# Kernel optimization log

Hardware: AMD Instinct MI355X
Metric: run time of the kernel (lower is better)

The kernel has to match this reference:

```python
import jax, jax.numpy as jnp
import numpy as np

ALPHA = 2.0  # init alpha
B, N, E = 8, 100000, 3200000


def setup_inputs() -> dict:
    key = jax.random.key(0)
    k1, k2, k3, k4 = jax.random.split(key, 4)
    y = jax.random.normal(k1, (B, N), dtype=jnp.float32)
    t = jnp.zeros((1,), dtype=jnp.float32)  # unused by the math, kept for signature fidelity
    graph_edge_attr = jax.random.uniform(k2, (E,), dtype=jnp.float32)
    dist_w = jax.random.normal(k3, (E,), dtype=jnp.float32)  # distances.weight ([E,1] flattened)
    edge_index = jax.random.randint(k4, (2, E), 0, N, dtype=jnp.int64)
    return {"y": y, "t": t, "graph_edge_attr": graph_edge_attr, "dist_w": dist_w, "edge_index": edge_index}


def reference(y, t, graph_edge_attr, dist_w, edge_index):
    ei0 = edge_index[0]  # source node per edge [E]
    ei1 = edge_index[1]  # target node per edge [E]
    n = y.shape[1]
    # edge_attr = sigmoid(distances.weight) -> [E]
    edge_attr = jax.nn.sigmoid(dist_w)
    # deg = scatter_add(graph.edge_attr, edge_index[0], dim_size=N) -> [N]
    deg = jax.ops.segment_sum(graph_edge_attr, ei0, num_segments=n)
    deg_a = jnp.power(deg[ei0], ALPHA)  # [E], gathered per edge at source node
    # grad_m = sqrt(edge_attr) * -1 * min(y[:,ei1]/deg^a - y[:,ei0]/deg^a, 0) -> [B,E]
    diff = y[:, ei1] / deg_a - y[:, ei0] / deg_a
    grad_m = jnp.sqrt(edge_attr) * (-1.0) * jnp.minimum(diff, 0.0)
    # grad_norm = scatter_add(|grad_m|, ei0, dim=1, dim_size=N) -> [B,N]
    grad_norm = jnp.zeros_like(y).at[:, ei0].add(jnp.abs(grad_m))
    # run_pde is None -> return f (mask branch not taken)
    return 1.0 - grad_norm
```

## Files before the change

kernel.cpp:

```cpp
#include <hip/hip_runtime.h>
#include <hip/hip_fp16.h>

#define BATCH 8
#define S_LOG 9
#define SBUCKET 512
#define KC 256
#define CB 1024
#define TTILE 2048
#define EPT 8
#define MA 8

static inline size_t alignup(size_t x) { return (x + 255) & ~(size_t)255; }

__device__ __forceinline__ unsigned bf16hi(unsigned u) {
    return (u + 0x7FFFu + ((u >> 16) & 1u)) >> 16;
}

__device__ __forceinline__ int aligned_chunk(int E) {
    return (((E + CB - 1) / CB) + 15) & ~15;
}


__global__ __launch_bounds__(256)
void count_transpose_kernel(const int* __restrict__ ei0, unsigned* __restrict__ counts,
                            const float* __restrict__ y, uint4* __restrict__ yT,
                            int E, int N, int Npad) {
    __shared__ unsigned cnt[KC];
    int tid = threadIdx.x;
    if (blockIdx.x >= CB) {
        int n = (blockIdx.x - CB) * 256 + tid;
        if (n < Npad) {
            uint4 o = make_uint4(0u, 0u, 0u, 0u);
            if (n < N) {
                unsigned p[8];
#pragma unroll
                for (int b = 0; b < BATCH; ++b)
                    p[b] = bf16hi(__float_as_uint(y[(size_t)b * N + n]));
                o = make_uint4(p[0] | (p[1] << 16), p[2] | (p[3] << 16),
                               p[4] | (p[5] << 16), p[6] | (p[7] << 16));
            }
            yT[n] = o;
        }
        return;
    }
    cnt[tid] = 0;
    __syncthreads();
    int chunk = aligned_chunk(E);
    int lo = blockIdx.x * chunk;
    int hi = min(lo + chunk, E);
    for (int bi = lo; bi < hi; bi += 1024) {
        int idx = bi + tid * 4;
        if (idx + 4 <= hi) {
            int4 v = *(const int4*)(ei0 + idx);
            atomicAdd(&cnt[(unsigned)v.x >> S_LOG], 1u);
            atomicAdd(&cnt[(unsigned)v.y >> S_LOG], 1u);
            atomicAdd(&cnt[(unsigned)v.z >> S_LOG], 1u);
            atomicAdd(&cnt[(unsigned)v.w >> S_LOG], 1u);
        } else {
#pragma unroll
            for (int j = 0; j < 4; ++j) {
                int i2 = idx + j;
                if (i2 < hi) atomicAdd(&cnt[(unsigned)ei0[i2] >> S_LOG], 1u);
            }
        }
    }
    __syncthreads();
    counts[(size_t)tid * CB + blockIdx.x] = cnt[tid];
}

__global__ __launch_bounds__(256)
void scanB1_kernel(const unsigned* __restrict__ counts, unsigned* __restrict__ base,
                   unsigned* __restrict__ tot) {
    __shared__ unsigned ssum[256];
    int k = blockIdx.x, tid = threadIdx.x;
    const uint4* row4 = (const uint4*)(counts + (size_t)k * CB);
    uint4 v = row4[tid];
    unsigned lsum = v.x + v.y + v.z + v.w;
    ssum[tid] = lsum;
    __syncthreads();
    for (int off = 1; off < 256; off <<= 1) {
        unsigned u = ssum[tid];
        unsigned a = (tid >= off) ? ssum[tid - off] : 0u;
        __syncthreads();
        ssum[tid] = u + a;
        __syncthreads();
    }
    unsigned ex = ssum[tid] - lsum;
    if (tid == 255) tot[k] = ssum[255];
    uint4 o;
    o.x = ex;
    o.y = ex + v.x;
    o.z = o.y + v.y;
    o.w = o.z + v.z;
    ((uint4*)(base + (size_t)k * CB))[tid] = o;
}

__global__ void scanC_kernel(const unsigned* __restrict__ tot,
                             unsigned* __restrict__ bb, int E, int K) {
    __shared__ unsigned sb[KC];
    int t = threadIdx.x;
    unsigned v = (t < K) ? tot[t] : 0u;
    sb[t] = v;
    __syncthreads();
    for (int off = 1; off < KC; off <<= 1) {
        unsigned u = sb[t];
        unsigned a = (t >= off) ? sb[t - off] : 0u;
        __syncthreads();
        sb[t] = u + a;
        __syncthreads();
    }
    bb[t] = sb[t] - v;
    if (t == KC - 1) bb[KC] = (unsigned)E;
}

__global__ __launch_bounds__(256)
void scatter_kernel(const int* __restrict__ ei0, const int* __restrict__ ei1,
                    const float* __restrict__ dw, const float* __restrict__ gea,
                    const unsigned* __restrict__ base, const unsigned* __restrict__ bb,
                    uint2* __restrict__ w0coef, int E) {
    __shared__ unsigned cursor[KC];
    __shared__ unsigned h[KC];
    __shared__ unsigned tstart[KC];
    __shared__ unsigned wsum[4];
    __shared__ uint2 srec[TTILE];
    __shared__ unsigned char skey[TTILE];
    int tid = threadIdx.x;
    cursor[tid] = base[(size_t)tid * CB + blockIdx.x] + bb[tid];
    int chunk = aligned_chunk(E);
    int lo = blockIdx.x * chunk;
    int hi = min(lo + chunk, E);
    __syncthreads();

    for (int tileLo = lo; tileLo < hi; tileLo += TTILE) {
        int tn = min(TTILE, hi - tileLo);
        h[tid] = 0;
        __syncthreads();

        int base_off = tid * EPT;
        unsigned k_r[EPT], w0_r[EPT], pk_r[EPT], rk_r[EPT];
        int s0a[EPT], s1a[EPT];
        float dwa[EPT], gea_a[EPT];
        bool anyv = base_off < tn;
        if (base_off + EPT <= tn) {
            const int4* p0 = (const int4*)(ei0 + tileLo + base_off);
            const int4* p1 = (const int4*)(ei1 + tileLo + base_off);
            const float4* pd = (const float4*)(dw + tileLo + base_off);
            const float4* pg = (const float4*)(gea + tileLo + base_off);
            int4 a0 = p0[0], a1 = p0[1];
            int4 b0 = p1[0], b1 = p1[1];
            float4 d0 = pd[0], d1 = pd[1];
            float4 g0 = pg[0], g1 = pg[1];
            s0a[0]=a0.x; s0a[1]=a0.y; s0a[2]=a0.z; s0a[3]=a0.w;
            s0a[4]=a1.x; s0a[5]=a1.y; s0a[6]=a1.z; s0a[7]=a1.w;
            s1a[0]=b0.x; s1a[1]=b0.y; s1a[2]=b0.z; s1a[3]=b0.w;
            s1a[4]=b1.x; s1a[5]=b1.y; s1a[6]=b1.z; s1a[7]=b1.w;
            dwa[0]=d0.x; dwa[1]=d0.y; dwa[2]=d0.z; dwa[3]=d0.w;
            dwa[4]=d1.x; dwa[5]=d1.y; dwa[6]=d1.z; dwa[7]=d1.w;
            gea_a[0]=g0.x; gea_a[1]=g0.y; gea_a[2]=g0.z; gea_a[3]=g0.w;
            gea_a[4]=g1.x; gea_a[5]=g1.y; gea_a[6]=g1.z; gea_a[7]=g1.w;
#pragma unroll
            for (int j = 0; j < EPT; ++j) k_r[j] = 0u;
#pragma unroll
            for (int j = 0; j < EPT; ++j) {
                unsigned k = (unsigned)s0a[j] >> S_LOG;
                unsigned s0l = (unsigned)(s0a[j] & (SBUCKET - 1));
                k_r[j] = k;
                w0_r[j] = (unsigned)s1a[j] | (s0l << 17);
                float sig = 1.0f / (1.0f + __expf(-dwa[j]));
                pk_r[j] = (bf16hi(__float_as_uint(sqrtf(sig))) << 16) |
                          bf16hi(__float_as_uint(gea_a[j]));
            }
#pragma unroll
            for (int j = 0; j < EPT; ++j)
                rk_r[j] = atomicAdd(&h[k_r[j]], 1u);
        } else {
#pragma unroll
            for (int j = 0; j < EPT; ++j) {
                int off = base_off + j;
                k_r[j] = 0xFFFFFFFFu;
                if (off < tn) {
                    int i = tileLo + off;
                    int s0v = ei0[i];
                    int s1v = ei1[i];
                    unsigned k = (unsigned)s0v >> S_LOG;
                    unsigned s0l = (unsigned)(s0v & (SBUCKET - 1));
                    k_r[j] = k;
                    w0_r[j] = (unsigned)s1v | (s0l << 17);
                    float sig = 1.0f / (1.0f + __expf(-dw[i]));
                    pk_r[j] = (bf16hi(__float_as_uint(sqrtf(sig))) << 16) |
                              bf16hi(__float_as_uint(gea[i]));
                }
            }
#pragma unroll
            for (int j = 0; j < EPT; ++j)
                if (k_r[j] != 0xFFFFFFFFu) rk_r[j] = atomicAdd(&h[k_r[j]], 1u);
        }
        bool fullv = base_off + EPT <= tn;
        __syncthreads();

        unsigned hv = h[tid];
        unsigned v = hv;
        unsigned lane = tid & 63;
        unsigned wv = tid >> 6;
#pragma unroll
        for (int off = 1; off < 64; off <<= 1) {
            unsigned t = __shfl_up(v, off, 64);
            if (lane >= off) v += t;
        }
        if (lane == 63) wsum[wv] = v;
        __syncthreads();
        unsigned addv = 0;
#pragma unroll
        for (unsigned w = 0; w < 4; ++w)
            if (w < wv) addv += wsum[w];
        tstart[tid] = v + addv - hv;
        __syncthreads();

        if (fullv) {
#pragma unroll
            for (int j = 0; j < EPT; ++j) {
                unsigned slot = tstart[k_r[j]] + rk_r[j];
                srec[slot] = make_uint2(w0_r[j], pk_r[j]);
                skey[slot] = (unsigned char)k_r[j];
            }
        } else if (anyv) {
#pragma unroll
            for (int j = 0; j < EPT; ++j)
                if (k_r[j] != 0xFFFFFFFFu) {
                    unsigned slot = tstart[k_r[j]] + rk_r[j];
                    srec[slot] = make_uint2(w0_r[j], pk_r[j]);
                    skey[slot] = (unsigned char)k_r[j];
                }
        }
        __syncthreads();

        for (int i = tid; i < tn; i += 256) {
            uint2 u = srec[i];
            unsigned k = skey[i];
            unsigned pos = cursor[k] + ((unsigned)i - tstart[k]);
            w0coef[pos] = u;
        }
        __syncthreads();
        cursor[tid] += h[tid];
        __syncthreads();
    }
}

__global__ __launch_bounds__(128)
void accum_kernel(const uint2* __restrict__ w0coef, const unsigned* __restrict__ bb,
                  const uint4* __restrict__ yT,
                  float* __restrict__ pdegp, __half2* __restrict__ pout,
                  int N, int Npad) {
    __shared__ uint4  outw[2][SBUCKET];
    __shared__ float  degw[2][SBUCKET];
    int k = blockIdx.x, m = blockIdx.y, tid = threadIdx.x;
    int n0 = k << S_LOG;
    unsigned lane = tid & 63;
    unsigned wv = tid >> 6;

    uint4 z4i = make_uint4(0u, 0u, 0u, 0u);
    for (int i = tid; i < 2 * SBUCKET; i += 128)
        ((uint4*)outw)[i] = z4i;
    for (int i = tid; i < 2 * SBUCKET; i += 128)
        ((float*)degw)[i] = 0.0f;
    unsigned lo = bb[k], hi = bb[k + 1];
    unsigned cnt = hi - lo;
    unsigned slice = (cnt + MA - 1) / MA;
    unsigned slo = lo + m * slice;
    unsigned shi = min(slo + slice, hi);
    __syncthreads();

    uint4* myout = outw[wv];
    float* mydeg = degw[wv];

    unsigned i0 = slo + tid;
    uint2 z2 = make_uint2(0u, 0u);
    uint2 c0 = z2, c1 = z2, d0 = z2, d1 = z2;
    uint4 zg = make_uint4(0u, 0u, 0u, 0u);
    uint4 g0 = zg, g1 = zg, yg0 = zg, yg1 = zg;
    bool vc0 = i0 < shi,       vc1 = i0 + 128 < shi;
    bool vd0 = i0 + 256 < shi, vd1 = i0 + 384 < shi;
    if (vc0) c0 = w0coef[i0];
    if (vc1) c1 = w0coef[i0 + 128];
    if (vd0) d0 = w0coef[i0 + 256];
    if (vd1) d1 = w0coef[i0 + 384];
    if (vc0) { g0 = yT[c0.x & 0x1FFFFu]; yg0 = yT[n0 + (c0.x >> 17)]; }
    if (vc1) { g1 = yT[c1.x & 0x1FFFFu]; yg1 = yT[n0 + (c1.x >> 17)]; }

    while (__any(vc0)) {
        uint4 h0 = zg, h1 = zg, yh0 = zg, yh1 = zg;
        if (vd0) { h0 = yT[d0.x & 0x1FFFFu]; yh0 = yT[n0 + (d0.x >> 17)]; }
        if (vd1) { h1 = yT[d1.x & 0x1FFFFu]; yh1 = yT[n0 + (d1.x >> 17)]; }
        uint2 e0 = z2, e1 = z2;
        bool ve0 = i0 + 512 < shi, ve1 = i0 + 640 < shi;
        if (ve0) e0 = w0coef[i0 + 512];
        if (ve1) e1 = w0coef[i0 + 640];

#pragma unroll
        for (int half = 0; half < 2; ++half) {
            bool val = half ? vc1 : vc0;
            uint2 cc = half ? c1 : c0;
            uint4 gg = half ? g1 : g0;
            uint4 y0r = half ? yg1 : yg0;
            unsigned s0l = cc.x >> 17;
            unsigned long long mm = ~0ull;
#pragma unroll
            for (int b = 0; b < 9; ++b) {
                unsigned long long vb = __ballot((s0l >> b) & 1u);
                mm &= ((s0l >> b) & 1u) ? vb : ~vb;
            }
            unsigned rank = __popcll(mm & ((1ull << lane) - 1ull));
            float cf = __uint_as_float(cc.y & 0xFFFF0000u);
            float ge = __uint_as_float(cc.y << 16);
            float q[8];
            {
                const unsigned yw[4] = {y0r.x, y0r.y, y0r.z, y0r.w};
                const unsigned gw[4] = {gg.x, gg.y, gg.z, gg.w};
#pragma unroll
                for (int p = 0; p < 4; ++p) {
                    float ya = __uint_as_float(yw[p] << 16);
                    float yb = __uint_as_float(yw[p] & 0xFFFF0000u);
                    float ga = __uint_as_float(gw[p] << 16);
                    float gb = __uint_as_float(gw[p] & 0xFFFF0000u);
                    q[2 * p]     = cf * fmaxf(ya - ga, 0.0f);
                    q[2 * p + 1] = cf * fmaxf(yb - gb, 0.0f);
                }
            }
            unsigned r = 0;
            bool pending = val;
            while (__any(pending && rank >= r ? 1 : 0)) {
                if (pending && rank == r) {
                    uint4 cur = myout[s0l];
                    unsigned cw[4] = {cur.x, cur.y, cur.z, cur.w};
#pragma unroll
                    for (int p = 0; p < 4; ++p) {
                        __half2 hv = *reinterpret_cast<__half2*>(&cw[p]);
                        float2 f = __half22float2(hv);
                        f.x += q[2 * p];
                        f.y += q[2 * p + 1];
                        hv = __floats2half2_rn(f.x, f.y);
                        cw[p] = *reinterpret_cast<unsigned*>(&hv);
                    }
                    myout[s0l] = make_uint4(cw[0], cw[1], cw[2], cw[3]);
                    mydeg[s0l] += ge;
                    pending = false;
                }
                ++r;
            }
        }

        c0 = d0; c1 = d1; d0 = e0; d1 = e1;
        g0 = h0; g1 = h1; yg0 = yh0; yg1 = yh1;
        vc0 = vd0; vc1 = vd1; vd0 = ve0; vd1 = ve1;
        i0 += 256;
    }
    __syncthreads();

    for (int i = tid; i < SBUCKET; i += 128)
        pdegp[(size_t)m * Npad + n0 + i] = degw[0][i] + degw[1][i];
    for (int j = tid; j < SBUCKET; j += 128) {
        uint4 a = outw[0][j];
        uint4 b = outw[1][j];
        unsigned aw[4] = {a.x, a.y, a.z, a.w};
        unsigned bw[4] = {b.x, b.y, b.z, b.w};
#pragma unroll
        for (int p = 0; p < 4; ++p) {
            float2 fa = __half22float2(*reinterpret_cast<__half2*>(&aw[p]));
            float2 fb = __half22float2(*reinterpret_cast<__half2*>(&bw[p]));
            pout[((size_t)m * 4 + p) * Npad + n0 + j] =
                __floats2half2_rn(fa.x + fb.x, fa.y + fb.y);
        }
    }
}

__global__ __launch_bounds__(256)
void finalize_kernel(const float* __restrict__ pdegp, const __half2* __restrict__ pout,
                     float* __restrict__ out, int N, int Npad) {
    int n = blockIdx.x * blockDim.x + threadIdx.x;
    if (n >= N) return;
    float d = 0.0f;
#pragma unroll
    for (int m = 0; m < MA; ++m) d += pdegp[(size_t)m * Npad + n];
    float inv = 1.0f / (d * d);
#pragma unroll
    for (int p = 0; p < 4; ++p) {
        float sx = 0.0f, sy = 0.0f;
#pragma unroll
        for (int m = 0; m < MA; ++m) {
            float2 f = __half22float2(pout[((size_t)m * 4 + p) * Npad + n]);
            sx += f.x; sy += f.y;
        }
        out[(size_t)(2 * p) * N + n]     = 1.0f - sx * inv;
        out[(size_t)(2 * p + 1) * N + n] = 1.0f - sy * inv;
    }
}


__global__ void fill_one_kernel(float* __restrict__ out, int n) {
    int i = blockIdx.x * blockDim.x + threadIdx.x;
    if (i < n) out[i] = 1.0f;
}

__global__ void zero_kernel(float* __restrict__ p, int n) {
    int i = blockIdx.x * blockDim.x + threadIdx.x;
    if (i < n) p[i] = 0.0f;
}

__global__ void deg_kernel(const float* __restrict__ gea,
                           const int* __restrict__ ei0,
                           float* __restrict__ deg, int E) {
    int e = blockIdx.x * blockDim.x + threadIdx.x;
    if (e < E) atomicAdd(&deg[ei0[e]], gea[e]);
}

__global__ void edge_kernel(const float* __restrict__ y,
                            const float* __restrict__ dw,
                            const int* __restrict__ ei0,
                            const int* __restrict__ ei1,
                            const float* __restrict__ deg,
                            float* __restrict__ out,
                            int E, int N) {
    int e = blockIdx.x * blockDim.x + threadIdx.x;
    if (e >= E) return;
    int s0 = ei0[e];
    int s1 = ei1[e];
    float d = deg[s0];
    float inv = 1.0f / (d * d);
    float sig = 1.0f / (1.0f + __expf(-dw[e]));
    float coef = sqrtf(sig) * inv;
#pragma unroll
    for (int b = 0; b < BATCH; ++b) {
        float y0 = y[(size_t)b * N + s0];
        float y1 = y[(size_t)b * N + s1];
        float gm = coef * fmaxf(y0 - y1, 0.0f);
        if (gm != 0.0f) atomicAdd(&out[(size_t)b * N + s0], -gm);
    }
}


extern "C" void kernel_launch(void* const* d_in, const int* in_sizes, int n_in,
                              void* d_out, int out_size, void* d_ws, size_t ws_size,
                              hipStream_t stream) {
    const float* y   = (const float*)d_in[0];
    const float* gea = (const float*)d_in[2];
    const float* dw  = (const float*)d_in[3];
    const int*   ei  = (const int*)d_in[4];

    const int E = in_sizes[2];
    const int N = in_sizes[0] / BATCH;
    const int* ei0 = ei;
    const int* ei1 = ei + E;

    const int K = (N + SBUCKET - 1) >> S_LOG;
    const int Npad = K << S_LOG;

    size_t o_yT     = 0;
    size_t o_rcf    = o_yT     + alignup((size_t)Npad * 16);
    size_t o_counts = o_rcf    + alignup((size_t)E * 8);
    size_t o_base   = o_counts + alignup((size_t)KC * CB * 4);
    size_t o_tot    = o_base   + alignup((size_t)KC * CB * 4);
    size_t o_bb     = o_tot    + alignup((size_t)KC * 4);
    size_t o_pdegp  = o_bb     + alignup((size_t)(KC + 1) * 4);
    size_t o_pout   = o_pdegp  + alignup((size_t)MA * Npad * 4);
    size_t need     = o_pout   + alignup((size_t)MA * 4 * Npad * 4);

    if (K <= KC && N <= 131071 && ws_size >= need) {
        char* w = (char*)d_ws;
        uint4*    yT     = (uint4*)(w + o_yT);
        uint2*    w0coef = (uint2*)(w + o_rcf);
        unsigned* counts = (unsigned*)(w + o_counts);
        unsigned* base   = (unsigned*)(w + o_base);
        unsigned* tot    = (unsigned*)(w + o_tot);
        unsigned* bb     = (unsigned*)(w + o_bb);
        float*    pdegp  = (float*)(w + o_pdegp);
        __half2*  pout   = (__half2*)(w + o_pout);

        int tb = (Npad + 255) / 256;
        count_transpose_kernel<<<CB + tb, 256, 0, stream>>>(ei0, counts, y, yT,
                                                            E, N, Npad);
        scanB1_kernel<<<K, 256, 0, stream>>>(counts, base, tot);
        scanC_kernel<<<1, KC, 0, stream>>>(tot, bb, E, K);
        scatter_kernel<<<CB, 256, 0, stream>>>(ei0, ei1, dw, gea, base, bb,
                                               w0coef, E);
        accum_kernel<<<dim3(K, MA), 128, 0, stream>>>(w0coef, bb, yT,
                                                      pdegp, pout, N, Npad);
        finalize_kernel<<<(N + 255) / 256, 256, 0, stream>>>(
            pdegp, pout, (float*)d_out, N, Npad);
    } else {
        float* deg = (float*)d_ws;
        zero_kernel<<<(N + 255) / 256, 256, 0, stream>>>(deg, N);
        fill_one_kernel<<<(out_size + 255) / 256, 256, 0, stream>>>((float*)d_out, out_size);
        deg_kernel<<<(E + 255) / 256, 256, 0, stream>>>(gea, ei0, deg, E);
        edge_kernel<<<(E + 255) / 256, 256, 0, stream>>>(y, dw, ei0, ei1, deg,
                                                         (float*)d_out, E, N);
    }
}
```

Baseline: 159.9 us.

## Defer duplicate-slot updates to shared overflow queue instead of serialized rank loop

In the per-bucket accumulation loop, only the first lane targeting each slot updates shared memory directly. Lanes that collide are pushed into a per-wave shared overflow queue and processed in batches later with the rank-serialized path, which re-gathers yT for them. This removes the wave-wide serialization loop from the common path at the cost of extra LDS, atomics and re-gathers for duplicates. MA is also reduced from 8 to 6, giving fewer edge slices per bucket.

```diff
diff --git a/kernel.cpp b/kernel.cpp
--- a/kernel.cpp
+++ b/kernel.cpp
@@ -8,7 +8,8 @@
 #define CB 1024
 #define TTILE 2048
 #define EPT 8
-#define MA 8
+#define MA 6
+#define QCAP 384
 
 static inline size_t alignup(size_t x) { return (x + 255) & ~(size_t)255; }
 
@@ -246,6 +247,61 @@
     }
 }
 
+__device__ __forceinline__ void process_dups(uint4* myout, float* mydeg,
+                                             const uint4* __restrict__ yT, int n0,
+                                             uint2 cc, bool val, unsigned lane) {
+    unsigned s0l = cc.x >> 17;
+    unsigned long long mm = ~0ull;
+#pragma unroll
+    for (int b = 0; b < 9; ++b) {
+        unsigned long long vb = __ballot((s0l >> b) & 1u);
+        mm &= ((s0l >> b) & 1u) ? vb : ~vb;
+    }
+    {
+        unsigned long long vb = __ballot(val ? 1 : 0);
+        mm &= val ? vb : ~vb;
+    }
+    unsigned rank = __popcll(mm & ((1ull << lane) - 1ull));
+    uint4 zg = make_uint4(0u, 0u, 0u, 0u);
+    uint4 gg = zg, y0r = zg;
+    if (val) { gg = yT[cc.x & 0x1FFFFu]; y0r = yT[n0 + s0l]; }
+    float cf = __uint_as_float(cc.y & 0xFFFF0000u);
+    float ge = __uint_as_float(cc.y << 16);
+    float q[8];
+    const unsigned yw[4] = {y0r.x, y0r.y, y0r.z, y0r.w};
+    const unsigned gw[4] = {gg.x, gg.y, gg.z, gg.w};
+#pragma unroll
+    for (int p = 0; p < 4; ++p) {
+        float ya = __uint_as_float(yw[p] << 16);
+        float yb = __uint_as_float(yw[p] & 0xFFFF0000u);
+        float ga = __uint_as_float(gw[p] << 16);
+        float gb = __uint_as_float(gw[p] & 0xFFFF0000u);
+        q[2 * p]     = cf * fmaxf(ya - ga, 0.0f);
+        q[2 * p + 1] = cf * fmaxf(yb - gb, 0.0f);
+    }
+    unsigned r = 0;
+    bool pending = val;
+    while (__any(pending && rank >= r ? 1 : 0)) {
+        if (pending && rank == r) {
+            uint4 cur = myout[s0l];
+            unsigned cw[4] = {cur.x, cur.y, cur.z, cur.w};
+#pragma unroll
+            for (int p = 0; p < 4; ++p) {
+                __half2 hv = *reinterpret_cast<__half2*>(&cw[p]);
+                float2 f = __half22float2(hv);
+                f.x += q[2 * p];
+                f.y += q[2 * p + 1];
+                hv = __floats2half2_rn(f.x, f.y);
+                cw[p] = *reinterpret_cast<unsigned*>(&hv);
+            }
+            myout[s0l] = make_uint4(cw[0], cw[1], cw[2], cw[3]);
+            mydeg[s0l] += ge;
+            pending = false;
+        }
+        ++r;
+    }
+}
+
 __global__ __launch_bounds__(128)
 void accum_kernel(const uint2* __restrict__ w0coef, const unsigned* __restrict__ bb,
                   const uint4* __restrict__ yT,
@@ -253,6 +309,8 @@
                   int N, int Npad) {
     __shared__ uint4  outw[2][SBUCKET];
     __shared__ float  degw[2][SBUCKET];
+    __shared__ uint2  ovq[2][QCAP];
+    __shared__ unsigned ovn[2];
     int k = blockIdx.x, m = blockIdx.y, tid = threadIdx.x;
     int n0 = k << S_LOG;
     unsigned lane = tid & 63;
@@ -263,6 +321,7 @@
         ((uint4*)outw)[i] = z4i;
     for (int i = tid; i < 2 * SBUCKET; i += 128)
         ((float*)degw)[i] = 0.0f;
+    if (tid < 2) ovn[tid] = 0u;
     unsigned lo = bb[k], hi = bb[k + 1];
     unsigned cnt = hi - lo;
     unsigned slice = (cnt + MA - 1) / MA;
@@ -288,6 +347,16 @@
     if (vc1) { g1 = yT[c1.x & 0x1FFFFu]; yg1 = yT[n0 + (c1.x >> 17)]; }
 
     while (__any(vc0)) {
+        if (ovn[wv] > (QCAP - 130)) {
+            unsigned qn = ovn[wv];
+            for (unsigned qb = 0; qb < qn; qb += 64) {
+                unsigned qidx = qb + lane;
+                uint2 qc = (qidx < qn) ? ovq[wv][qidx] : z2;
+                process_dups(myout, mydeg, yT, n0, qc, qidx < qn, lane);
+            }
+            if (lane == 0) ovn[wv] = 0u;
+        }
+
         uint4 h0 = zg, h1 = zg, yh0 = zg, yh1 = zg;
         if (vd0) { h0 = yT[d0.x & 0x1FFFFu]; yh0 = yT[n0 + (d0.x >> 17)]; }
         if (vd1) { h1 = yT[d1.x & 0x1FFFFu]; yh1 = yT[n0 + (d1.x >> 17)]; }
@@ -309,27 +378,27 @@
                 unsigned long long vb = __ballot((s0l >> b) & 1u);
                 mm &= ((s0l >> b) & 1u) ? vb : ~vb;
             }
+            {
+                unsigned long long vb = __ballot(val ? 1 : 0);
+                mm &= val ? vb : ~vb;
+            }
             unsigned rank = __popcll(mm & ((1ull << lane) - 1ull));
-            float cf = __uint_as_float(cc.y & 0xFFFF0000u);
-            float ge = __uint_as_float(cc.y << 16);
-            float q[8];
-            {
-                const unsigned yw[4] = {y0r.x, y0r.y, y0r.z, y0r.w};
-                const unsigned gw[4] = {gg.x, gg.y, gg.z, gg.w};
-#pragma unroll
-                for (int p = 0; p < 4; ++p) {
-                    float ya = __uint_as_float(yw[p] << 16);
-                    float yb = __uint_as_float(yw[p] & 0xFFFF0000u);
-                    float ga = __uint_as_float(gw[p] << 16);
-                    float gb = __uint_as_float(gw[p] & 0xFFFF0000u);
-                    q[2 * p]     = cf * fmaxf(ya - ga, 0.0f);
-                    q[2 * p + 1] = cf * fmaxf(yb - gb, 0.0f);
-                }
-            }
-            unsigned r = 0;
-            bool pending = val;
-            while (__any(pending && rank >= r ? 1 : 0)) {
-                if (pending && rank == r) {
+            if (val) {
+                if (rank == 0) {
+                    float cf = __uint_as_float(cc.y & 0xFFFF0000u);
+                    float ge = __uint_as_float(cc.y << 16);
+                    const unsigned yw[4] = {y0r.x, y0r.y, y0r.z, y0r.w};
+                    const unsigned gw[4] = {gg.x, gg.y, gg.z, gg.w};
+                    float q[8];
+#pragma unroll
+                    for (int p = 0; p < 4; ++p) {
+                        float ya = __uint_as_float(yw[p] << 16);
+                        float yb = __uint_as_float(yw[p] & 0xFFFF0000u);
+                        float ga = __uint_as_float(gw[p] << 16);
+                        float gb = __uint_as_float(gw[p] & 0xFFFF0000u);
+                        q[2 * p]     = cf * fmaxf(ya - ga, 0.0f);
+                        q[2 * p + 1] = cf * fmaxf(yb - gb, 0.0f);
+                    }
                     uint4 cur = myout[s0l];
                     unsigned cw[4] = {cur.x, cur.y, cur.z, cur.w};
 #pragma unroll
@@ -343,9 +412,10 @@
                     }
                     myout[s0l] = make_uint4(cw[0], cw[1], cw[2], cw[3]);
                     mydeg[s0l] += ge;
-                    pending = false;
+                } else {
+                    unsigned qi = atomicAdd(&ovn[wv], 1u);
+                    ovq[wv][qi] = cc;
                 }
-                ++r;
             }
         }
 
@@ -353,6 +423,15 @@
         g0 = h0; g1 = h1; yg0 = yh0; yg1 = yh1;
         vc0 = vd0; vc1 = vd1; vd0 = ve0; vd1 = ve1;
         i0 += 256;
+    }
+
+    {
+        unsigned qn = ovn[wv];
+        for (unsigned qb = 0; qb < qn; qb += 64) {
+            unsigned qidx = qb + lane;
+            uint2 qc = (qidx < qn) ? ovq[wv][qidx] : z2;
+            process_dups(myout, mydeg, yT, n0, qc, qidx < qn, lane);
+        }
     }
     __syncthreads();
 
```

Measured after the change: 157.3 us. No clear change (-1.6%).
